# Optimization experiments

Measured on AMD Instinct MI355X. Metric: run time of the kernel, lower is better.

Reference implementation:

```python
import jax, jax.numpy as jnp
import numpy as np

EPS = 1e-5
H = 16  # num_heads

def layer_norm(x, g, b):
    mu = jnp.mean(x, axis=-1, keepdims=True)
    var = jnp.mean(jnp.square(x - mu), axis=-1, keepdims=True)
    return (x - mu) * jax.lax.rsqrt(var + EPS) * g + b

def setup_inputs() -> dict:
    key = jax.random.key(0)
    ks = jax.random.split(key, 12)
    B, N, D, F = 4, 1024, 1024, 4096
    s = 0.02
    return {
        'x': jax.random.normal(ks[0], (B, N, D), jnp.float32),
        'ln1_g': jnp.ones((D,), jnp.float32), 'ln1_b': jnp.zeros((D,), jnp.float32),
        'Wq': s * jax.random.normal(ks[1], (D, D), jnp.float32), 'bq': jnp.zeros((D,), jnp.float32),
        'Wk': s * jax.random.normal(ks[2], (D, D), jnp.float32), 'bk': jnp.zeros((D,), jnp.float32),
        'Wv': s * jax.random.normal(ks[3], (D, D), jnp.float32), 'bv': jnp.zeros((D,), jnp.float32),
        'Wo': s * jax.random.normal(ks[4], (D, D), jnp.float32), 'bo': jnp.zeros((D,), jnp.float32),
        'ln2_g': jnp.ones((D,), jnp.float32), 'ln2_b': jnp.zeros((D,), jnp.float32),
        'W1': s * jax.random.normal(ks[5], (D, F), jnp.float32), 'b1': jnp.zeros((F,), jnp.float32),
        'W2': s * jax.random.normal(ks[6], (F, D), jnp.float32), 'b2': jnp.zeros((D,), jnp.float32),
        'pad_mask': jnp.zeros((B, N), jnp.bool_),
    }

def reference(x, ln1_g, ln1_b, Wq, bq, Wk, bk, Wv, bv, Wo, bo,
              ln2_g, ln2_b, W1, b1, W2, b2, pad_mask):
    B, N, D = x.shape
    c = D // H  # per-head channels
    h = layer_norm(x, ln1_g, ln1_b)
    q = (h @ Wq + bq).reshape(B, N, H, c).transpose(0, 2, 1, 3)  # b h n c
    k = (h @ Wk + bk).reshape(B, N, H, c).transpose(0, 2, 1, 3)
    v = (h @ Wv + bv).reshape(B, N, H, c).transpose(0, 2, 1, 3)
    q = q * (c ** -0.5)
    attn = jnp.einsum('bhic,bhjc->bhij', q, k)
    neg = -jnp.finfo(attn.dtype).max
    attn = jnp.where(pad_mask[:, None, None, :], neg, attn)
    causal = jnp.triu(jnp.ones((N, N), jnp.bool_), k=1)  # right-aligned, i==j
    attn = jnp.where(causal, neg, attn)
    attn = jax.nn.softmax(attn, axis=-1)
    o = jnp.einsum('bhij,bhjc->bhic', attn, v)
    o = o.transpose(0, 2, 1, 3).reshape(B, N, D)
    x = o @ Wo + bo + x  # attention residual
    m = layer_norm(x, ln2_g, ln2_b)
    m = jax.nn.gelu(m @ W1 + b1, approximate=False) @ W2 + b2
    return x + m
```

## Files before the change

### kernel.cpp

```cpp
#include <hip/hip_runtime.h>
#include <hip/hip_bf16.h>
#include <cmath>

typedef __bf16 bf16_t;
typedef __bf16 bf16x8 __attribute__((ext_vector_type(8)));
typedef __bf16 bf16x4 __attribute__((ext_vector_type(4)));
typedef float f32x4 __attribute__((ext_vector_type(4)));

#define AS1 __attribute__((address_space(1)))
#define AS3 __attribute__((address_space(3)))

__device__ __forceinline__ void async_lds16(const void* g, void* s) {
    __builtin_amdgcn_global_load_lds((const AS1 void*)g, (AS3 void*)s, 16, 0, 0);
}

__global__ __launch_bounds__(256) void k_transpose_bf16(
    const float* __restrict__ src, bf16_t* __restrict__ dst, int R, int C) {
    __shared__ float tile[32][33];
    const int tx = threadIdx.x & 31, ty = threadIdx.x >> 5;
    const int r0 = blockIdx.y << 5, c0 = blockIdx.x << 5;
#pragma unroll
    for (int i = 0; i < 32; i += 8)
        tile[ty + i][tx] = src[(size_t)(r0 + ty + i) * C + c0 + tx];
    __syncthreads();
#pragma unroll
    for (int i = 0; i < 32; i += 8)
        dst[(size_t)(c0 + ty + i) * R + r0 + tx] = (bf16_t)tile[tx][ty + i];
}

__global__ __launch_bounds__(256) void k_layernorm(
    const float* __restrict__ x, const float* __restrict__ g,
    const float* __restrict__ b, bf16_t* __restrict__ out) {
    const int row = blockIdx.x;
    const int t = threadIdx.x;
    const float4 xv = reinterpret_cast<const float4*>(x + (size_t)row * 1024)[t];
    float s = xv.x + xv.y + xv.z + xv.w;
    float s2 = xv.x * xv.x + xv.y * xv.y + xv.z * xv.z + xv.w * xv.w;
#pragma unroll
    for (int mk = 32; mk >= 1; mk >>= 1) {
        s += __shfl_xor(s, mk);
        s2 += __shfl_xor(s2, mk);
    }
    __shared__ float red[8];
    const int w = t >> 6, l = t & 63;
    if (l == 0) { red[w] = s; red[4 + w] = s2; }
    __syncthreads();
    s = red[0] + red[1] + red[2] + red[3];
    s2 = red[4] + red[5] + red[6] + red[7];
    const float mu = s * (1.0f / 1024.0f);
    const float var = s2 * (1.0f / 1024.0f) - mu * mu;
    const float rs = rsqrtf(var + 1e-5f);
    const float4 gv = reinterpret_cast<const float4*>(g)[t];
    const float4 bv = reinterpret_cast<const float4*>(b)[t];
    bf16x4 o4;
    o4[0] = (bf16_t)((xv.x - mu) * rs * gv.x + bv.x);
    o4[1] = (bf16_t)((xv.y - mu) * rs * gv.y + bv.y);
    o4[2] = (bf16_t)((xv.z - mu) * rs * gv.z + bv.z);
    o4[3] = (bf16_t)((xv.w - mu) * rs * gv.w + bv.w);
    *reinterpret_cast<bf16x4*>(out + (size_t)row * 1024 + t * 4) = o4;
}

__global__ __launch_bounds__(256) void k_reduce_ln(
    const float* __restrict__ p0, const float* __restrict__ p1,
    const float* __restrict__ bo, const float* __restrict__ x,
    const float* __restrict__ g, const float* __restrict__ b,
    float* __restrict__ x2, bf16_t* __restrict__ m2) {
    const int row = blockIdx.x;
    const int t = threadIdx.x;
    const size_t off = (size_t)row * 1024;
    const float4 a0 = reinterpret_cast<const float4*>(p0 + off)[t];
    const float4 a1 = reinterpret_cast<const float4*>(p1 + off)[t];
    const float4 bb = reinterpret_cast<const float4*>(bo)[t];
    const float4 xv = reinterpret_cast<const float4*>(x + off)[t];
    float4 v;
    v.x = a0.x + a1.x + bb.x + xv.x;
    v.y = a0.y + a1.y + bb.y + xv.y;
    v.z = a0.z + a1.z + bb.z + xv.z;
    v.w = a0.w + a1.w + bb.w + xv.w;
    reinterpret_cast<float4*>(x2 + off)[t] = v;
    float s = v.x + v.y + v.z + v.w;
    float s2 = v.x * v.x + v.y * v.y + v.z * v.z + v.w * v.w;
#pragma unroll
    for (int mk = 32; mk >= 1; mk >>= 1) {
        s += __shfl_xor(s, mk);
        s2 += __shfl_xor(s2, mk);
    }
    __shared__ float red[8];
    const int w = t >> 6, l = t & 63;
    if (l == 0) { red[w] = s; red[4 + w] = s2; }
    __syncthreads();
    s = red[0] + red[1] + red[2] + red[3];
    s2 = red[4] + red[5] + red[6] + red[7];
    const float mu = s * (1.0f / 1024.0f);
    const float var = s2 * (1.0f / 1024.0f) - mu * mu;
    const float rs = rsqrtf(var + 1e-5f);
    const float4 gv = reinterpret_cast<const float4*>(g)[t];
    const float4 bv = reinterpret_cast<const float4*>(b)[t];
    bf16x4 o4;
    o4[0] = (bf16_t)((v.x - mu) * rs * gv.x + bv.x);
    o4[1] = (bf16_t)((v.y - mu) * rs * gv.y + bv.y);
    o4[2] = (bf16_t)((v.z - mu) * rs * gv.z + bv.z);
    o4[3] = (bf16_t)((v.w - mu) * rs * gv.w + bv.w);
    *reinterpret_cast<bf16x4*>(m2 + off + t * 4) = o4;
}

__global__ __launch_bounds__(256) void k_reduce_out(
    const float* __restrict__ pA, const float* __restrict__ pB,
    const float* __restrict__ b2, const float* __restrict__ x2,
    float* __restrict__ outp) {
    const size_t i = (size_t)blockIdx.x * 256 + threadIdx.x;
    const float4 a = reinterpret_cast<const float4*>(pA)[i];
    const float4 b = reinterpret_cast<const float4*>(pB)[i];
    const float4 c = reinterpret_cast<const float4*>(x2)[i];
    const float4 bi = reinterpret_cast<const float4*>(b2)[i & 255];
    float4 v;
    v.x = a.x + b.x + c.x + bi.x;
    v.y = a.y + b.y + c.y + bi.y;
    v.z = a.z + b.z + c.z + bi.z;
    v.w = a.w + b.w + c.w + bi.w;
    reinterpret_cast<float4*>(outp)[i] = v;
}

enum { EPI_QKV = 0, EPI_GELU = 1, EPI_PART = 2 };

template <int EPI>
__global__ __launch_bounds__(256, 3) void k_gemm2(
    const bf16_t* __restrict__ A, const bf16_t* __restrict__ BT,
    const float* __restrict__ bias0, const float* __restrict__ bias1,
    const float* __restrict__ bias2,
    float* __restrict__ outF, bf16_t* __restrict__ outB,
    bf16_t* __restrict__ outB2, bf16_t* __restrict__ outB3,
    int M, int N, int Ksub, int Kstr, long long zstride) {
    const int gx = gridDim.x;
    const int nwg = gx * gridDim.y;
    int lin = blockIdx.y * gx + blockIdx.x;
    if ((nwg & 7) == 0) lin = (lin & 7) * (nwg >> 3) + (lin >> 3);
    const int mbase = (lin / gx) * 128;
    const int nbase = (lin % gx) * 128;

    const bf16_t* Ab = A + (size_t)blockIdx.z * Ksub;
    const bf16_t* Bb = BT + (size_t)blockIdx.z * Ksub;
    float* poutF = outF;
    if constexpr (EPI == EPI_PART) poutF = outF + (size_t)blockIdx.z * zstride;

    const int t = threadIdx.x;
    const int w = t >> 6, l = t & 63;
    const int wr = w >> 1, wc = w & 1;
    const int lrow = l & 15, lg = l >> 4;

    __shared__ alignas(16) bf16_t As[3][128 * 32];
    __shared__ alignas(16) bf16_t Bs[3][128 * 32];

    f32x4 acc[4][4] = {};

    const int sr = t >> 2;
    const int sc = t & 3;
    const int ssw = (sc ^ ((sr >> 1) & 3)) * 8;

    auto stage = [&](int ks, int buf) {
        const int k0 = ks << 5;
#pragma unroll
        for (int c = 0; c < 2; c++)
            async_lds16(Ab + (size_t)(mbase + c * 64 + sr) * Kstr + k0 + ssw,
                        &As[buf][c * 2048 + t * 8]);
#pragma unroll
        for (int c = 0; c < 2; c++)
            async_lds16(Bb + (size_t)(nbase + c * 64 + sr) * Kstr + k0 + ssw,
                        &Bs[buf][c * 2048 + t * 8]);
    };

    stage(0, 0);
    stage(1, 1);
    const int nt = Ksub >> 5;
    int cur = 0;
    for (int tt = 0; tt < nt; tt++) {
        asm volatile("s_waitcnt vmcnt(4)" ::: "memory");
        __builtin_amdgcn_sched_barrier(0);
        __builtin_amdgcn_s_barrier();
        __builtin_amdgcn_sched_barrier(0);
        if (tt + 2 < nt) {
            int nb = cur + 2; if (nb >= 3) nb -= 3;
            stage(tt + 2, nb);
        }
        bf16x8 a[4], b[4];
#pragma unroll
        for (int i = 0; i < 4; i++) {
            const int r = wr * 64 + i * 16 + lrow;
            a[i] = *reinterpret_cast<const bf16x8*>(
                &As[cur][r * 32 + ((lg ^ ((r >> 1) & 3)) * 8)]);
        }
#pragma unroll
        for (int j = 0; j < 4; j++) {
            const int r = wc * 64 + j * 16 + lrow;
            b[j] = *reinterpret_cast<const bf16x8*>(
                &Bs[cur][r * 32 + ((lg ^ ((r >> 1) & 3)) * 8)]);
        }
        __builtin_amdgcn_s_setprio(1);
#pragma unroll
        for (int i = 0; i < 4; i++)
#pragma unroll
            for (int j = 0; j < 4; j++)
                acc[i][j] = __builtin_amdgcn_mfma_f32_16x16x32_bf16(a[i], b[j], acc[i][j], 0, 0, 0);
        __builtin_amdgcn_s_setprio(0);
        cur = cur + 1; if (cur >= 3) cur = 0;
    }

#pragma unroll
    for (int i = 0; i < 4; i++) {
#pragma unroll
        for (int j = 0; j < 4; j++) {
            const int col = nbase + wc * 64 + j * 16 + lrow;
            float bj = 0.f;
            int kind = 0, cc = col;
            if constexpr (EPI == EPI_QKV) {
                kind = col >> 10; cc = col & 1023;
                bj = (kind == 0 ? bias0 : kind == 1 ? bias1 : bias2)[cc];
            } else if constexpr (EPI == EPI_GELU) {
                bj = bias0[col];
            }
#pragma unroll
            for (int r = 0; r < 4; r++) {
                const int row = mbase + wr * 64 + i * 16 + lg * 4 + r;
                const float v = acc[i][j][r] + bj;
                if constexpr (EPI == EPI_QKV) {
                    const int bidx = row >> 10, ns = row & 1023;
                    const int hh = cc >> 6, ch = cc & 63;
                    const int bhh = bidx * 16 + hh;
                    if (kind == 0)
                        outB[((size_t)bhh * 1024 + ns) * 64 + ch] = (bf16_t)(v * 0.125f);
                    else if (kind == 1)
                        outB2[((size_t)bhh * 1024 + ns) * 64 + ch] = (bf16_t)v;
                    else
                        outB3[((size_t)bhh * 64 + ch) * 1024 + ns] = (bf16_t)v;
                } else if constexpr (EPI == EPI_GELU) {
                    const float ge = 0.5f * v * (1.0f + erff(v * 0.70710678118654752f));
                    outB[(size_t)row * N + col] = (bf16_t)ge;
                } else {
                    poutF[(size_t)row * N + col] = v;
                }
            }
        }
    }
}

__global__ __launch_bounds__(256, 4) void k_attn(
    const bf16_t* __restrict__ q, const bf16_t* __restrict__ kk,
    const bf16_t* __restrict__ vt, const unsigned char* __restrict__ pad,
    bf16_t* __restrict__ o) {
    const int qt = 15 - (blockIdx.x >> 6);
    const int bh = blockIdx.x & 63;
    const int bb = bh >> 4, hh = bh & 15;
    const int t = threadIdx.x;
    const int w = t >> 6, l = t & 63;
    const int lrow = l & 15, lg = l >> 4;
    const int qbase = qt * 64;

    __shared__ alignas(16) bf16_t Ks[64 * 64];
    __shared__ alignas(16) bf16_t Vs[64 * 64];
    __shared__ alignas(16) bf16_t Ps[4][16 * 64];

    const size_t bh_off = (size_t)bh * 1024 * 64;
    const int qrow = qbase + w * 16 + lrow;
    bf16x8 qf[2];
#pragma unroll
    for (int ks = 0; ks < 2; ks++)
        qf[ks] = *reinterpret_cast<const bf16x8*>(q + bh_off + (size_t)qrow * 64 + ks * 32 + lg * 8);

    f32x4 oacc[4] = {};
    float mrow[4] = {-1e30f, -1e30f, -1e30f, -1e30f};
    float lsum[4] = {0.f, 0.f, 0.f, 0.f};

    const int sr = t >> 3;
    const int ssw = ((t & 7) ^ (sr & 7)) * 8;

    for (int kb = 0; kb < qbase + 64; kb += 64) {
        __syncthreads();
        const bf16_t* kp = kk + bh_off + (size_t)kb * 64;
        async_lds16(kp + (size_t)sr * 64 + ssw, Ks + t * 8);
        async_lds16(kp + (size_t)(32 + sr) * 64 + ssw, Ks + 2048 + t * 8);
        const bf16_t* vp = vt + bh_off + kb;
        async_lds16(vp + (size_t)sr * 1024 + ssw, Vs + t * 8);
        async_lds16(vp + (size_t)(32 + sr) * 1024 + ssw, Vs + 2048 + t * 8);
        __syncthreads();

        f32x4 s[4] = {};
#pragma unroll
        for (int ks = 0; ks < 2; ks++) {
#pragma unroll
            for (int jt = 0; jt < 4; jt++) {
                const int kr = jt * 16 + lrow;
                bf16x8 bfr = *reinterpret_cast<const bf16x8*>(
                    Ks + kr * 64 + (((ks * 4 + lg) ^ (kr & 7)) * 8));
                s[jt] = __builtin_amdgcn_mfma_f32_16x16x32_bf16(qf[ks], bfr, s[jt], 0, 0, 0);
            }
        }
#pragma unroll
        for (int jt = 0; jt < 4; jt++) {
            const int kvg = kb + jt * 16 + lrow;
            const bool padm = pad[bb * 1024 + kvg] != 0;
#pragma unroll
            for (int r = 0; r < 4; r++) {
                const int qg = qbase + w * 16 + lg * 4 + r;
                if (kvg > qg || padm) s[jt][r] = -1e30f;
            }
        }
        float alpha[4];
#pragma unroll
        for (int r = 0; r < 4; r++) {
            float mx = fmaxf(fmaxf(s[0][r], s[1][r]), fmaxf(s[2][r], s[3][r]));
#pragma unroll
            for (int mk = 8; mk >= 1; mk >>= 1) mx = fmaxf(mx, __shfl_xor(mx, mk));
            const float mn = fmaxf(mrow[r], mx);
            alpha[r] = __expf(mrow[r] - mn);
            mrow[r] = mn;
        }
#pragma unroll
        for (int jt = 0; jt < 4; jt++)
#pragma unroll
            for (int r = 0; r < 4; r++)
                s[jt][r] = __expf(s[jt][r] - mrow[r]);
#pragma unroll
        for (int r = 0; r < 4; r++) {
            float sm = s[0][r] + s[1][r] + s[2][r] + s[3][r];
#pragma unroll
            for (int mk = 8; mk >= 1; mk >>= 1) sm += __shfl_xor(sm, mk);
            lsum[r] = lsum[r] * alpha[r] + sm;
        }
#pragma unroll
        for (int ct = 0; ct < 4; ct++)
#pragma unroll
            for (int r = 0; r < 4; r++)
                oacc[ct][r] *= alpha[r];
#pragma unroll
        for (int jt = 0; jt < 4; jt++)
#pragma unroll
            for (int r = 0; r < 4; r++) {
                const int prow = lg * 4 + r;
                const int kvc = jt * 16 + lrow;
                Ps[w][prow * 64 + (((kvc >> 3) ^ (prow & 7)) * 8) + (kvc & 7)] = (bf16_t)s[jt][r];
            }
#pragma unroll
        for (int ks = 0; ks < 2; ks++) {
            bf16x8 pa = *reinterpret_cast<const bf16x8*>(
                &Ps[w][lrow * 64 + (((ks * 4 + lg) ^ (lrow & 7)) * 8)]);
#pragma unroll
            for (int ct = 0; ct < 4; ct++) {
                const int vr = ct * 16 + lrow;
                bf16x8 vb = *reinterpret_cast<const bf16x8*>(
                    Vs + vr * 64 + (((ks * 4 + lg) ^ (vr & 7)) * 8));
                oacc[ct] = __builtin_amdgcn_mfma_f32_16x16x32_bf16(pa, vb, oacc[ct], 0, 0, 0);
            }
        }
    }
#pragma unroll
    for (int ct = 0; ct < 4; ct++) {
#pragma unroll
        for (int r = 0; r < 4; r++) {
            const int qg = qbase + w * 16 + lg * 4 + r;
            const float val = oacc[ct][r] / lsum[r];
            o[((size_t)bb * 1024 + qg) * 1024 + hh * 64 + ct * 16 + lrow] = (bf16_t)val;
        }
    }
}

extern "C" void kernel_launch(void* const* d_in, const int* in_sizes, int n_in,
                              void* d_out, int out_size, void* d_ws, size_t ws_size,
                              hipStream_t stream) {
    const float* x    = (const float*)d_in[0];
    const float* ln1g = (const float*)d_in[1];
    const float* ln1b = (const float*)d_in[2];
    const float* Wq   = (const float*)d_in[3];
    const float* bq   = (const float*)d_in[4];
    const float* Wk   = (const float*)d_in[5];
    const float* bk   = (const float*)d_in[6];
    const float* Wv   = (const float*)d_in[7];
    const float* bv   = (const float*)d_in[8];
    const float* Wo   = (const float*)d_in[9];
    const float* bo   = (const float*)d_in[10];
    const float* ln2g = (const float*)d_in[11];
    const float* ln2b = (const float*)d_in[12];
    const float* W1   = (const float*)d_in[13];
    const float* b1   = (const float*)d_in[14];
    const float* W2   = (const float*)d_in[15];
    const float* b2   = (const float*)d_in[16];
    const unsigned char* pad = (const unsigned char*)d_in[17];

    char* ws = (char*)d_ws;
    const size_t MB = 1024 * 1024;
    bf16_t* WqkvT = (bf16_t*)(ws + 0 * MB);
    bf16_t* WoT = (bf16_t*)(ws + 6 * MB);
    bf16_t* W1T = (bf16_t*)(ws + 8 * MB);
    bf16_t* W2T = (bf16_t*)(ws + 16 * MB);
    bf16_t* h   = (bf16_t*)(ws + 24 * MB);
    bf16_t* qb  = (bf16_t*)(ws + 32 * MB);
    bf16_t* kb  = (bf16_t*)(ws + 40 * MB);
    bf16_t* vb  = (bf16_t*)(ws + 48 * MB);
    bf16_t* ob  = (bf16_t*)(ws + 56 * MB);
    float*  ppO = (float*)(ws + 24 * MB);
    float*  x2  = (float*)(ws + 56 * MB);
    bf16_t* m2  = (bf16_t*)(ws + 72 * MB);
    bf16_t* hid = (bf16_t*)(ws + 24 * MB);
    float*  ppW0 = (float*)(ws + 0 * MB);
    float*  ppW1 = (float*)(ws + 80 * MB);

    const dim3 blk(256);
    k_transpose_bf16<<<dim3(32, 32), blk, 0, stream>>>(Wq, WqkvT, 1024, 1024);
    k_transpose_bf16<<<dim3(32, 32), blk, 0, stream>>>(Wk, WqkvT + 1024 * 1024, 1024, 1024);
    k_transpose_bf16<<<dim3(32, 32), blk, 0, stream>>>(Wv, WqkvT + 2048 * 1024, 1024, 1024);
    k_transpose_bf16<<<dim3(32, 32), blk, 0, stream>>>(Wo, WoT, 1024, 1024);
    k_transpose_bf16<<<dim3(128, 32), blk, 0, stream>>>(W1, W1T, 1024, 4096);
    k_transpose_bf16<<<dim3(32, 128), blk, 0, stream>>>(W2, W2T, 4096, 1024);
    k_layernorm<<<4096, blk, 0, stream>>>(x, ln1g, ln1b, h);
    k_gemm2<EPI_QKV><<<dim3(24, 32), blk, 0, stream>>>(
        h, WqkvT, bq, bk, bv, nullptr, qb, kb, vb, 4096, 3072, 1024, 1024, 0);
    k_attn<<<1024, blk, 0, stream>>>(qb, kb, vb, pad, ob);
    k_gemm2<EPI_PART><<<dim3(8, 32, 2), blk, 0, stream>>>(
        ob, WoT, nullptr, nullptr, nullptr, ppO, nullptr, nullptr, nullptr,
        4096, 1024, 512, 1024, 4096ll * 1024);
    k_reduce_ln<<<4096, blk, 0, stream>>>(ppO, ppO + 4096ll * 1024, bo, x,
                                          ln2g, ln2b, x2, m2);
    k_gemm2<EPI_GELU><<<dim3(32, 32), blk, 0, stream>>>(
        m2, W1T, b1, nullptr, nullptr, nullptr, hid, nullptr, nullptr,
        4096, 4096, 1024, 1024, 0);
    k_gemm2<EPI_PART><<<dim3(8, 32, 2), blk, 0, stream>>>(
        hid, W2T, nullptr, nullptr, nullptr, ppW0, nullptr, nullptr, nullptr,
        4096, 1024, 2048, 4096, 20ll * 1024 * 1024);
    k_reduce_out<<<4096, blk, 0, stream>>>(ppW0, ppW1, b2, x2, (float*)d_out);
}
```

Baseline: 258.5 us.

## Use split-K of four with bf16 partials and double-buffered GEMM pipeline

The Wo and W2 GEMMs now split K four ways instead of two, and write their partial sums in bf16 rather than fp32. The reduce kernels are rewritten to sum four bf16 partials. The GEMM drops from triple to double buffering with a full vmcnt(0) wait, and launch bounds rise from 3 to 5 waves per SIMD. The intent is more workgroups and occupancy for the narrow N=1024 GEMMs plus less partial-sum traffic, at the cost of precision loss in the bf16 partials and less load latency hiding in the GEMM loop.

```diff
diff --git a/kernel.cpp b/kernel.cpp
--- a/kernel.cpp
+++ b/kernel.cpp
@@ -12,6 +12,10 @@
 
 __device__ __forceinline__ void async_lds16(const void* g, void* s) {
     __builtin_amdgcn_global_load_lds((const AS1 void*)g, (AS3 void*)s, 16, 0, 0);
+}
+
+__device__ __forceinline__ float bf2f(bf16_t v) {
+    return (float)v;
 }
 
 __global__ __launch_bounds__(256) void k_transpose_bf16(
@@ -60,24 +64,24 @@
     *reinterpret_cast<bf16x4*>(out + (size_t)row * 1024 + t * 4) = o4;
 }
 
-__global__ __launch_bounds__(256) void k_reduce_ln(
-    const float* __restrict__ p0, const float* __restrict__ p1,
+__global__ __launch_bounds__(256) void k_reduce_ln4(
+    const bf16_t* __restrict__ pp,
     const float* __restrict__ bo, const float* __restrict__ x,
     const float* __restrict__ g, const float* __restrict__ b,
-    float* __restrict__ x2, bf16_t* __restrict__ m2) {
+    float* __restrict__ x2, bf16_t* __restrict__ m2, long long zs) {
     const int row = blockIdx.x;
     const int t = threadIdx.x;
-    const size_t off = (size_t)row * 1024;
-    const float4 a0 = reinterpret_cast<const float4*>(p0 + off)[t];
-    const float4 a1 = reinterpret_cast<const float4*>(p1 + off)[t];
+    const size_t off = (size_t)row * 1024 + t * 4;
     const float4 bb = reinterpret_cast<const float4*>(bo)[t];
-    const float4 xv = reinterpret_cast<const float4*>(x + off)[t];
+    const float4 xv = *reinterpret_cast<const float4*>(x + off);
     float4 v;
-    v.x = a0.x + a1.x + bb.x + xv.x;
-    v.y = a0.y + a1.y + bb.y + xv.y;
-    v.z = a0.z + a1.z + bb.z + xv.z;
-    v.w = a0.w + a1.w + bb.w + xv.w;
-    reinterpret_cast<float4*>(x2 + off)[t] = v;
+    v.x = bb.x + xv.x; v.y = bb.y + xv.y; v.z = bb.z + xv.z; v.w = bb.w + xv.w;
+#pragma unroll
+    for (int z = 0; z < 4; z++) {
+        const bf16x4 p = *reinterpret_cast<const bf16x4*>(pp + z * zs + off);
+        v.x += bf2f(p[0]); v.y += bf2f(p[1]); v.z += bf2f(p[2]); v.w += bf2f(p[3]);
+    }
+    *reinterpret_cast<float4*>(x2 + off) = v;
     float s = v.x + v.y + v.z + v.w;
     float s2 = v.x * v.x + v.y * v.y + v.z * v.z + v.w * v.w;
 #pragma unroll
@@ -101,35 +105,39 @@
     o4[1] = (bf16_t)((v.y - mu) * rs * gv.y + bv.y);
     o4[2] = (bf16_t)((v.z - mu) * rs * gv.z + bv.z);
     o4[3] = (bf16_t)((v.w - mu) * rs * gv.w + bv.w);
-    *reinterpret_cast<bf16x4*>(m2 + off + t * 4) = o4;
-}
-
-__global__ __launch_bounds__(256) void k_reduce_out(
-    const float* __restrict__ pA, const float* __restrict__ pB,
+    *reinterpret_cast<bf16x4*>(m2 + off) = o4;
+}
+
+__global__ __launch_bounds__(256) void k_reduce_out4(
+    const bf16_t* __restrict__ pA, const bf16_t* __restrict__ pB,
     const float* __restrict__ b2, const float* __restrict__ x2,
-    float* __restrict__ outp) {
-    const size_t i = (size_t)blockIdx.x * 256 + threadIdx.x;
-    const float4 a = reinterpret_cast<const float4*>(pA)[i];
-    const float4 b = reinterpret_cast<const float4*>(pB)[i];
-    const float4 c = reinterpret_cast<const float4*>(x2)[i];
-    const float4 bi = reinterpret_cast<const float4*>(b2)[i & 255];
+    float* __restrict__ outp, long long zs) {
+    const size_t off = ((size_t)blockIdx.x * 256 + threadIdx.x) * 4;
+    const float4 c = *reinterpret_cast<const float4*>(x2 + off);
+    const float4 bi = reinterpret_cast<const float4*>(b2)[(off >> 2) & 255];
     float4 v;
-    v.x = a.x + b.x + c.x + bi.x;
-    v.y = a.y + b.y + c.y + bi.y;
-    v.z = a.z + b.z + c.z + bi.z;
-    v.w = a.w + b.w + c.w + bi.w;
-    reinterpret_cast<float4*>(outp)[i] = v;
-}
-
-enum { EPI_QKV = 0, EPI_GELU = 1, EPI_PART = 2 };
+    v.x = c.x + bi.x; v.y = c.y + bi.y; v.z = c.z + bi.z; v.w = c.w + bi.w;
+#pragma unroll
+    for (int z = 0; z < 2; z++) {
+        const bf16x4 a = *reinterpret_cast<const bf16x4*>(pA + z * zs + off);
+        const bf16x4 b = *reinterpret_cast<const bf16x4*>(pB + z * zs + off);
+        v.x += bf2f(a[0]) + bf2f(b[0]);
+        v.y += bf2f(a[1]) + bf2f(b[1]);
+        v.z += bf2f(a[2]) + bf2f(b[2]);
+        v.w += bf2f(a[3]) + bf2f(b[3]);
+    }
+    *reinterpret_cast<float4*>(outp + off) = v;
+}
+
+enum { EPI_QKV = 0, EPI_GELU = 1, EPI_PARTB = 2 };
 
 template <int EPI>
-__global__ __launch_bounds__(256, 3) void k_gemm2(
+__global__ __launch_bounds__(256, 5) void k_gemm2(
     const bf16_t* __restrict__ A, const bf16_t* __restrict__ BT,
     const float* __restrict__ bias0, const float* __restrict__ bias1,
     const float* __restrict__ bias2,
-    float* __restrict__ outF, bf16_t* __restrict__ outB,
-    bf16_t* __restrict__ outB2, bf16_t* __restrict__ outB3,
+    bf16_t* __restrict__ outB, bf16_t* __restrict__ outB2,
+    bf16_t* __restrict__ outB3,
     int M, int N, int Ksub, int Kstr, long long zstride) {
     const int gx = gridDim.x;
     const int nwg = gx * gridDim.y;
@@ -138,18 +146,13 @@
     const int mbase = (lin / gx) * 128;
     const int nbase = (lin % gx) * 128;
 
-    const bf16_t* Ab = A + (size_t)blockIdx.z * Ksub;
-    const bf16_t* Bb = BT + (size_t)blockIdx.z * Ksub;
-    float* poutF = outF;
-    if constexpr (EPI == EPI_PART) poutF = outF + (size_t)blockIdx.z * zstride;
-
     const int t = threadIdx.x;
     const int w = t >> 6, l = t & 63;
     const int wr = w >> 1, wc = w & 1;
     const int lrow = l & 15, lg = l >> 4;
 
-    __shared__ alignas(16) bf16_t As[3][128 * 32];
-    __shared__ alignas(16) bf16_t Bs[3][128 * 32];
+    __shared__ alignas(16) bf16_t As[2][128 * 32];
+    __shared__ alignas(16) bf16_t Bs[2][128 * 32];
 
     f32x4 acc[4][4] = {};
 
@@ -157,31 +160,28 @@
     const int sc = t & 3;
     const int ssw = (sc ^ ((sr >> 1) & 3)) * 8;
 
-    auto stage = [&](int ks, int buf) {
-        const int k0 = ks << 5;
-#pragma unroll
-        for (int c = 0; c < 2; c++)
-            async_lds16(Ab + (size_t)(mbase + c * 64 + sr) * Kstr + k0 + ssw,
-                        &As[buf][c * 2048 + t * 8]);
-#pragma unroll
-        for (int c = 0; c < 2; c++)
-            async_lds16(Bb + (size_t)(nbase + c * 64 + sr) * Kstr + k0 + ssw,
-                        &Bs[buf][c * 2048 + t * 8]);
+    const bf16_t* pa0 = A + (size_t)blockIdx.z * Ksub + (size_t)(mbase + sr) * Kstr + ssw;
+    const bf16_t* pa1 = pa0 + (size_t)64 * Kstr;
+    const bf16_t* pb0 = BT + (size_t)blockIdx.z * Ksub + (size_t)(nbase + sr) * Kstr + ssw;
+    const bf16_t* pb1 = pb0 + (size_t)64 * Kstr;
+
+    auto stage = [&](int kt, int buf) {
+        const int k0 = kt << 5;
+        async_lds16(pa0 + k0, &As[buf][t * 8]);
+        async_lds16(pa1 + k0, &As[buf][2048 + t * 8]);
+        async_lds16(pb0 + k0, &Bs[buf][t * 8]);
+        async_lds16(pb1 + k0, &Bs[buf][2048 + t * 8]);
     };
 
     stage(0, 0);
-    stage(1, 1);
     const int nt = Ksub >> 5;
-    int cur = 0;
     for (int tt = 0; tt < nt; tt++) {
-        asm volatile("s_waitcnt vmcnt(4)" ::: "memory");
+        const int cur = tt & 1;
+        asm volatile("s_waitcnt vmcnt(0)" ::: "memory");
         __builtin_amdgcn_sched_barrier(0);
         __builtin_amdgcn_s_barrier();
         __builtin_amdgcn_sched_barrier(0);
-        if (tt + 2 < nt) {
-            int nb = cur + 2; if (nb >= 3) nb -= 3;
-            stage(tt + 2, nb);
-        }
+        if (tt + 1 < nt) stage(tt + 1, cur ^ 1);
         bf16x8 a[4], b[4];
 #pragma unroll
         for (int i = 0; i < 4; i++) {
@@ -202,7 +202,6 @@
             for (int j = 0; j < 4; j++)
                 acc[i][j] = __builtin_amdgcn_mfma_f32_16x16x32_bf16(a[i], b[j], acc[i][j], 0, 0, 0);
         __builtin_amdgcn_s_setprio(0);
-        cur = cur + 1; if (cur >= 3) cur = 0;
     }
 
 #pragma unroll
@@ -236,7 +235,9 @@
                     const float ge = 0.5f * v * (1.0f + erff(v * 0.70710678118654752f));
                     outB[(size_t)row * N + col] = (bf16_t)ge;
                 } else {
-                    poutF[(size_t)row * N + col] = v;
+                    bf16_t* po = (blockIdx.z < 2 ? outB : outB2) +
+                                 (size_t)(blockIdx.z & 1) * zstride;
+                    po[(size_t)row * N + col] = (bf16_t)v;
                 }
             }
         }
@@ -396,12 +397,14 @@
     bf16_t* kb  = (bf16_t*)(ws + 40 * MB);
     bf16_t* vb  = (bf16_t*)(ws + 48 * MB);
     bf16_t* ob  = (bf16_t*)(ws + 56 * MB);
-    float*  ppO = (float*)(ws + 24 * MB);
-    float*  x2  = (float*)(ws + 56 * MB);
-    bf16_t* m2  = (bf16_t*)(ws + 72 * MB);
+    bf16_t* ppO = (bf16_t*)(ws + 24 * MB);
+    bf16_t* m2  = (bf16_t*)(ws + 56 * MB);
+    float*  x2  = (float*)(ws + 64 * MB);
     bf16_t* hid = (bf16_t*)(ws + 24 * MB);
-    float*  ppW0 = (float*)(ws + 0 * MB);
-    float*  ppW1 = (float*)(ws + 80 * MB);
+    bf16_t* pW01 = (bf16_t*)(ws + 0 * MB);
+    bf16_t* pW23 = (bf16_t*)(ws + 80 * MB);
+
+    const long long ZS = 4ll * 1024 * 1024;
 
     const dim3 blk(256);
     k_transpose_bf16<<<dim3(32, 32), blk, 0, stream>>>(Wq, WqkvT, 1024, 1024);
@@ -412,18 +415,17 @@
     k_transpose_bf16<<<dim3(32, 128), blk, 0, stream>>>(W2, W2T, 4096, 1024);
     k_layernorm<<<4096, blk, 0, stream>>>(x, ln1g, ln1b, h);
     k_gemm2<EPI_QKV><<<dim3(24, 32), blk, 0, stream>>>(
-        h, WqkvT, bq, bk, bv, nullptr, qb, kb, vb, 4096, 3072, 1024, 1024, 0);
+        h, WqkvT, bq, bk, bv, qb, kb, vb, 4096, 3072, 1024, 1024, 0);
     k_attn<<<1024, blk, 0, stream>>>(qb, kb, vb, pad, ob);
-    k_gemm2<EPI_PART><<<dim3(8, 32, 2), blk, 0, stream>>>(
-        ob, WoT, nullptr, nullptr, nullptr, ppO, nullptr, nullptr, nullptr,
-        4096, 1024, 512, 1024, 4096ll * 1024);
-    k_reduce_ln<<<4096, blk, 0, stream>>>(ppO, ppO + 4096ll * 1024, bo, x,
-                                          ln2g, ln2b, x2, m2);
+    k_gemm2<EPI_PARTB><<<dim3(8, 32, 4), blk, 0, stream>>>(
+        ob, WoT, nullptr, nullptr, nullptr, ppO, ppO + 2 * ZS, nullptr,
+        4096, 1024, 256, 1024, ZS);
+    k_reduce_ln4<<<4096, blk, 0, stream>>>(ppO, bo, x, ln2g, ln2b, x2, m2, ZS);
     k_gemm2<EPI_GELU><<<dim3(32, 32), blk, 0, stream>>>(
-        m2, W1T, b1, nullptr, nullptr, nullptr, hid, nullptr, nullptr,
+        m2, W1T, b1, nullptr, nullptr, hid, nullptr, nullptr,
         4096, 4096, 1024, 1024, 0);
-    k_gemm2<EPI_PART><<<dim3(8, 32, 2), blk, 0, stream>>>(
-        hid, W2T, nullptr, nullptr, nullptr, ppW0, nullptr, nullptr, nullptr,
-        4096, 1024, 2048, 4096, 20ll * 1024 * 1024);
-    k_reduce_out<<<4096, blk, 0, stream>>>(ppW0, ppW1, b2, x2, (float*)d_out);
-}
+    k_gemm2<EPI_PARTB><<<dim3(8, 32, 4), blk, 0, stream>>>(
+        hid, W2T, nullptr, nullptr, nullptr, pW01, pW23, nullptr,
+        4096, 1024, 1024, 4096, ZS);
+    k_reduce_out4<<<4096, blk, 0, stream>>>(pW01, pW23, b2, x2, (float*)d_out, ZS);
+}
```

After: 532.5 us. 2.06x slower.
